# Kernel tuning notes

Hardware: AMD Instinct MI355X
Metric: run time of the kernel (lower is better)

## Reference

```python
import jax, jax.numpy as jnp
import numpy as np

EMBED = 1024
NUM_HEADS = 16
HEAD = EMBED // NUM_HEADS  # 64


def setup_inputs() -> dict:
    key = jax.random.key(0)
    kx, kk, kq, kv = jax.random.split(key, 4)
    B, T = 4, 4096
    scale = 1.0 / np.sqrt(EMBED)
    x = jax.random.normal(kx, (B, T, EMBED), dtype=jnp.float32)
    # nn.Linear(embed, head, bias=False) stores weight [head, embed]
    Wk = jax.random.normal(kk, (HEAD, EMBED), dtype=jnp.float32) * scale
    Wq = jax.random.normal(kq, (HEAD, EMBED), dtype=jnp.float32) * scale
    Wv = jax.random.normal(kv, (HEAD, EMBED), dtype=jnp.float32) * scale
    return {"x": x, "Wk": Wk, "Wq": Wq, "Wv": Wv}


def reference(x, Wk, Wq, Wv):
    # x: [B, T, C]; W*: [H, C] (torch Linear layout, y = x @ W.T)
    k = jnp.einsum('btc,hc->bth', x, Wk)  # [B, T, H]
    q = jnp.einsum('btc,hc->bth', x, Wq)
    v = jnp.einsum('btc,hc->bth', x, Wv)
    scale = k.shape[-1] ** -0.5
    wei = jnp.einsum('bth,bsh->bts', q, k) * scale  # [B, T, T]
    wei = jax.nn.softmax(wei, axis=-1)  # no causal mask in source
    out = jnp.einsum('bts,bsh->bth', wei, v)  # [B, T, H]
    return out
```

## Files before the change

kernel.cpp:

```cpp
#include <hip/hip_runtime.h>
#include <hip/hip_bf16.h>
#include <cstdint>

#define TSEQ 4096
#define NB   4
#define HD   64
#define CEMB 1024
#define NQ   8
#define KVCH (TSEQ / NQ)
#define NTOK (NB * TSEQ)
#define SCL  0.18033688011112042f
#define FM   16.0f

typedef __attribute__((ext_vector_type(8)))  short bfrag;
typedef __attribute__((ext_vector_type(4)))  float f4;
typedef __attribute__((ext_vector_type(16))) float f16v;

#define MFMA16(a, b, c) __builtin_amdgcn_mfma_f32_16x16x32_bf16(a, b, c, 0, 0, 0)
#define MFMA32(a, b, c) __builtin_amdgcn_mfma_f32_32x32x16_bf16(a, b, c, 0, 0, 0)

static __device__ __forceinline__ unsigned short f2bf(float f) {
    __hip_bfloat16 h = __float2bfloat16(f);
    return __builtin_bit_cast(unsigned short, h);
}

static __device__ __forceinline__ float bf2f(unsigned short u) {
    const unsigned v = (unsigned)u << 16;
    return __builtin_bit_cast(float, v);
}

static __device__ __forceinline__ unsigned cvtpk(float lo, float hi) {
    unsigned r;
    asm("v_cvt_pk_bf16_f32 %0, %1, %2" : "=v"(r) : "v"(lo), "v"(hi));
    return r;
}

static __device__ __forceinline__ bfrag cvt8pk(const float4 a, const float4 b) {
    uint4 o;
    o.x = cvtpk(a.x, a.y);
    o.y = cvtpk(a.z, a.w);
    o.z = cvtpk(b.x, b.y);
    o.w = cvtpk(b.z, b.w);
    return __builtin_bit_cast(bfrag, o);
}


__global__ __launch_bounds__(256) void wcvt_kernel(
    const float* __restrict__ Wq, const float* __restrict__ Wk,
    const float* __restrict__ Wv, unsigned short* __restrict__ wb)
{
    const int row = blockIdx.x;
    const int col = threadIdx.x * 4;
    const float* W = (row < 64) ? Wq + (size_t)row * CEMB
                   : (row < 128) ? Wk + (size_t)(row - 64) * CEMB
                   : Wv + (size_t)(row - 128) * CEMB;
    const float4 v = *reinterpret_cast<const float4*>(W + col);
    ushort4 o;
    o.x = f2bf(v.x); o.y = f2bf(v.y); o.z = f2bf(v.z); o.w = f2bf(v.w);
    *reinterpret_cast<ushort4*>(wb + (size_t)row * CEMB + col) = o;
}

__global__ __launch_bounds__(256) void proj_kernel(
    const float* __restrict__ x, const unsigned short* __restrict__ wb,
    unsigned short* __restrict__ qb, unsigned short* __restrict__ kf,
    unsigned short* __restrict__ vf)
{
    __shared__ __attribute__((aligned(16))) unsigned short xs[2][32 * 64];
    __shared__ __attribute__((aligned(16))) unsigned short ws[2][192 * 64];

    const int tid  = threadIdx.x;
    const int w    = tid >> 6;
    const int lane = tid & 63;
    const int ln15 = lane & 15, lg = lane >> 4;
    const int rowg = (w >> 1) * 16;
    const int colg = (w & 1) * 96;
    const int rowbase = blockIdx.x * 32;

    f4 acc[6];
    #pragma unroll
    for (int j = 0; j < 6; ++j) acc[j] = f4{0.f, 0.f, 0.f, 0.f};

    const int xrow = tid >> 3;
    const int xs8  = tid & 7;
    const int xswz = (xrow & 7) << 4;

    float4 xf0, xf1;
    bfrag  wf[6];
    auto LOADP = [&](int k0) {
        const float* xsrc = x + (size_t)(rowbase + xrow) * CEMB + k0 + xs8 * 8;
        xf0 = reinterpret_cast<const float4*>(xsrc)[0];
        xf1 = reinterpret_cast<const float4*>(xsrc)[1];
        #pragma unroll
        for (int i = 0; i < 6; ++i) {
            const int seg = tid + i * 256;
            const int srow = seg >> 3, sc = seg & 7;
            wf[i] = *reinterpret_cast<const bfrag*>(wb + (size_t)srow * CEMB + k0 + sc * 8);
        }
    };
    auto WRITEP = [&](int c) {
        char* xd = (char*)xs[c];
        char* wd = (char*)ws[c];
        const bfrag xb = cvt8pk(xf0, xf1);
        *reinterpret_cast<bfrag*>(xd + xrow * 128 + ((xs8 * 16) ^ xswz)) = xb;
        #pragma unroll
        for (int i = 0; i < 6; ++i) {
            const int seg = tid + i * 256;
            const int srow = seg >> 3, sc = seg & 7;
            *reinterpret_cast<bfrag*>(wd + srow * 128 + ((sc * 16) ^ ((srow & 7) << 4))) = wf[i];
        }
    };

    LOADP(0);
    WRITEP(0);
    __syncthreads();

    for (int ch = 0; ch < 16; ++ch) {
        const int c = ch & 1;
        if (ch < 15) LOADP((ch + 1) * 64);

        const char* xp = (const char*)xs[c];
        const char* wp = (const char*)ws[c];
        __builtin_amdgcn_s_setprio(1);
        #pragma unroll
        for (int ks = 0; ks < 2; ++ks) {
            const int cb = ks * 64 + lg * 16;
            const int r0 = rowg + ln15;
            const bfrag a0 = *reinterpret_cast<const bfrag*>(xp + r0 * 128 + (cb ^ ((r0 & 7) << 4)));
            #pragma unroll
            for (int ct = 0; ct < 6; ++ct) {
                const int wr = colg + ct * 16 + ln15;
                const bfrag b = *reinterpret_cast<const bfrag*>(wp + wr * 128 + (cb ^ ((wr & 7) << 4)));
                acc[ct] = MFMA16(a0, b, acc[ct]);
            }
        }
        __builtin_amdgcn_s_setprio(0);

        if (ch < 15) WRITEP(c ^ 1);
        __syncthreads();
    }

    #pragma unroll
    for (int ct = 0; ct < 6; ++ct) {
        const int c = colg + ct * 16 + ln15;
        #pragma unroll
        for (int r = 0; r < 4; ++r) {
            const int grow = rowbase + rowg + 4 * lg + r;
            const int bbi = grow >> 12, t = grow & 4095;
            const int tile = t >> 6, kvr = t & 63;
            if (c < 64) {
                qb[(size_t)grow * HD + c] = f2bf(acc[ct][r] * SCL);
            } else if (c < 128) {
                const int d = c - 64;
                const unsigned short bv16 = f2bf(acc[ct][r]);
                const int lane2 = (kvr & 31) + 32 * ((d >> 3) & 1);
                const size_t idx =
                    ((((size_t)bbi * 64 + tile) * 4 + (d >> 4)) * 2 + (kvr >> 5)) * 512
                    + lane2 * 8 + (d & 7);
                kf[idx] = bv16;
            } else {
                const int d = c - 128;
                const unsigned short bv16 = f2bf(acc[ct][r]);
                const int lane2 = (d & 31) + 32 * ((kvr >> 3) & 1);
                const size_t idx =
                    ((((size_t)bbi * 64 + tile) * 4 + (kvr >> 4)) * 2 + (d >> 5)) * 512
                    + lane2 * 8 + (kvr & 7);
                vf[idx] = bv16;
            }
        }
    }
}

__global__ __launch_bounds__(256, 3) void attn_kernel(
    const unsigned short* __restrict__ qb, const unsigned short* __restrict__ kf,
    const unsigned short* __restrict__ vf, uint2* __restrict__ po2,
    float* __restrict__ pl)
{
    const int w    = threadIdx.x >> 6;
    const int lane = threadIdx.x & 63;
    const int ql   = lane & 31;
    const int hi   = lane >> 5;
    const int chunk = blockIdx.x;
    const int xg    = blockIdx.y;
    const int q0   = xg * 128 + w * 32;
    const int bb   = xg >> 5;
    const int tbase = bb * 64 + chunk * 8;

    bfrag aq[4];
    #pragma unroll
    for (int s = 0; s < 4; ++s)
        aq[s] = *reinterpret_cast<const bfrag*>(
            qb + (size_t)(q0 + ql) * HD + 16 * s + 8 * hi);

    const unsigned short* kp = kf + (size_t)tbase * 4096 + lane * 8;
    const unsigned short* vp = vf + (size_t)tbase * 4096 + lane * 8;

    bfrag ka[4], kc[4], va[4], vc[4];
    auto LOADK = [&](int it) {
        const unsigned short* p = kp + (size_t)it * 4096;
        #pragma unroll
        for (int s = 0; s < 4; ++s) {
            ka[s] = *reinterpret_cast<const bfrag*>(p + (2 * s) * 512);
            kc[s] = *reinterpret_cast<const bfrag*>(p + (2 * s + 1) * 512);
        }
    };
    auto LOADV = [&](int it) {
        const unsigned short* p = vp + (size_t)it * 4096;
        #pragma unroll
        for (int s = 0; s < 4; ++s) {
            va[s] = *reinterpret_cast<const bfrag*>(p + (2 * s) * 512);
            vc[s] = *reinterpret_cast<const bfrag*>(p + (2 * s + 1) * 512);
        }
    };

    auto mkpa = [&](const f16v& p, const int u0) -> bfrag {
        unsigned a0 = cvtpk(p[4 * u0 + 0], p[4 * u0 + 1]);
        unsigned a1 = cvtpk(p[4 * u0 + 2], p[4 * u0 + 3]);
        unsigned b0 = cvtpk(p[4 * u0 + 4], p[4 * u0 + 5]);
        unsigned b1 = cvtpk(p[4 * u0 + 6], p[4 * u0 + 7]);
        asm("v_permlane32_swap_b32 %0, %1" : "+v"(a0), "+v"(b0));
        asm("v_permlane32_swap_b32 %0, %1" : "+v"(a1), "+v"(b1));
        const uint4 u = make_uint4(a0, a1, b0, b1);
        return __builtin_bit_cast(bfrag, u);
    };

    f16v o0, o1;
    #pragma unroll
    for (int i = 0; i < 16; ++i) { o0[i] = 0.f; o1[i] = 0.f; }
    float lsum = 0.f;

    const int NIT = KVCH / 64;
    LOADK(0);
    LOADV(0);

    for (int it = 0; it < NIT; ++it) {
        f16v s0v, s1v;
        #pragma unroll
        for (int i = 0; i < 16; ++i) { s0v[i] = -FM; s1v[i] = -FM; }
        __builtin_amdgcn_s_setprio(1);
        #pragma unroll
        for (int s = 0; s < 4; ++s) {
            s0v = MFMA32(ka[s], aq[s], s0v);
            s1v = MFMA32(kc[s], aq[s], s1v);
        }
        __builtin_amdgcn_s_setprio(0);
        if (it < NIT - 1) LOADK(it + 1);

        #pragma unroll
        for (int i = 0; i < 16; ++i) {
            s0v[i] = __builtin_amdgcn_exp2f(s0v[i]);
            s1v[i] = __builtin_amdgcn_exp2f(s1v[i]);
        }
        float a[16];
        #pragma unroll
        for (int i = 0; i < 16; ++i) a[i] = s0v[i] + s1v[i];
        #pragma unroll
        for (int st = 8; st > 0; st >>= 1)
            #pragma unroll
            for (int i = 0; i < 8; ++i) if (i < st) a[i] += a[i + st];
        lsum += a[0];

        const bfrag pa0 = mkpa(s0v, 0);
        const bfrag pa1 = mkpa(s0v, 2);
        const bfrag pa2 = mkpa(s1v, 0);
        const bfrag pa3 = mkpa(s1v, 2);

        __builtin_amdgcn_s_setprio(1);
        o0 = MFMA32(va[0], pa0, o0);  o1 = MFMA32(vc[0], pa0, o1);
        o0 = MFMA32(va[1], pa1, o0);  o1 = MFMA32(vc[1], pa1, o1);
        o0 = MFMA32(va[2], pa2, o0);  o1 = MFMA32(vc[2], pa2, o1);
        o0 = MFMA32(va[3], pa3, o0);  o1 = MFMA32(vc[3], pa3, o1);
        __builtin_amdgcn_s_setprio(0);
        if (it < NIT - 1) LOADV(it + 1);
    }

    lsum += __shfl_xor(lsum, 32);

    const int wid = chunk * 512 + xg * 4 + w;
    uint2* pw = po2 + ((size_t)wid * 8) * 64 + lane;
    #pragma unroll
    for (int u = 0; u < 4; ++u) {
        uint2 w0, w1;
        w0.x = cvtpk(o0[4 * u + 0], o0[4 * u + 1]);
        w0.y = cvtpk(o0[4 * u + 2], o0[4 * u + 3]);
        pw[(size_t)u * 64] = w0;
        w1.x = cvtpk(o1[4 * u + 0], o1[4 * u + 1]);
        w1.y = cvtpk(o1[4 * u + 2], o1[4 * u + 3]);
        pw[(size_t)(4 + u) * 64] = w1;
    }
    if (hi == 0) {
        pl[chunk * NTOK + q0 + ql] = lsum;
    }
}

__global__ __launch_bounds__(256) void merge_kernel(
    const uint2* __restrict__ po2, const float* __restrict__ pl,
    float* __restrict__ out)
{
    const int t   = blockIdx.x * 256 + threadIdx.x;
    const int row = t >> 4, d0 = (t & 15) * 4;
    const int xg = row >> 7, w = (row >> 5) & 3, ql = row & 31;
    const int h = d0 >> 5, u = (d0 >> 3) & 3, hi = (d0 >> 2) & 1;
    const int lane = ql + 32 * hi;
    const int slot = h * 4 + u;

    float lt = 0.f;
    f4 acc = {0.f, 0.f, 0.f, 0.f};
    #pragma unroll
    for (int q = 0; q < NQ; ++q) {
        lt += pl[q * NTOK + row];
        const int wid = q * 512 + xg * 4 + w;
        const uint2 v = po2[((size_t)wid * 8 + slot) * 64 + lane];
        acc[0] += bf2f((unsigned short)(v.x & 0xffffu));
        acc[1] += bf2f((unsigned short)(v.x >> 16));
        acc[2] += bf2f((unsigned short)(v.y & 0xffffu));
        acc[3] += bf2f((unsigned short)(v.y >> 16));
    }
    const float inv = 1.0f / lt;
    f4 r = { acc[0] * inv, acc[1] * inv, acc[2] * inv, acc[3] * inv };
    *reinterpret_cast<f4*>(out + (size_t)row * HD + d0) = r;
}

extern "C" void kernel_launch(void* const* d_in, const int* in_sizes, int n_in,
                              void* d_out, int out_size, void* d_ws, size_t ws_size,
                              hipStream_t stream) {
    (void)in_sizes; (void)n_in; (void)out_size; (void)ws_size;
    const float* x  = (const float*)d_in[0];
    const float* Wk = (const float*)d_in[1];
    const float* Wq = (const float*)d_in[2];
    const float* Wv = (const float*)d_in[3];

    unsigned short* qb = (unsigned short*)d_ws;
    unsigned short* kf = qb + (size_t)NTOK * HD;
    unsigned short* vf = kf + (size_t)NTOK * HD;
    unsigned short* wb = vf + (size_t)NTOK * HD;
    uint2* po2 = (uint2*)(wb + (size_t)192 * CEMB);
    float* pl  = (float*)(po2 + (size_t)NQ * 512 * 8 * 64);

    wcvt_kernel<<<192, 256, 0, stream>>>(Wq, Wk, Wv, wb);
    proj_kernel<<<512, 256, 0, stream>>>(x, wb, qb, kf, vf);
    attn_kernel<<<dim3(NQ, 128), 256, 0, stream>>>(qb, kf, vf, po2, pl);
    merge_kernel<<<NTOK * HD / 1024, 256, 0, stream>>>(po2, pl, (float*)d_out);
}
```

Measured before the change: 57.81 us.

## Stage K/V tiles through double-buffered LDS shared across block waves

Previously each of the four waves in a block loaded the same K and V tile fragments straight from global memory into registers. Now the block loads each 64-key K/V tile once cooperatively, with each thread fetching a quarter, stores it into a double-buffered LDS array, and every wave reads its MFMA operands from LDS. This cuts redundant global and L2 traffic by a factor of four. In exchange it adds two block barriers per iteration and LDS reads in the inner loop, which may serialize waves and limit latency hiding.

```diff
diff --git a/kernel.cpp b/kernel.cpp
--- a/kernel.cpp
+++ b/kernel.cpp
@@ -175,8 +175,12 @@
     const unsigned short* __restrict__ vf, uint2* __restrict__ po2,
     float* __restrict__ pl)
 {
-    const int w    = threadIdx.x >> 6;
-    const int lane = threadIdx.x & 63;
+    __shared__ __attribute__((aligned(16))) unsigned short kl[2][4096];
+    __shared__ __attribute__((aligned(16))) unsigned short vl[2][4096];
+
+    const int tid  = threadIdx.x;
+    const int w    = tid >> 6;
+    const int lane = tid & 63;
     const int ql   = lane & 31;
     const int hi   = lane >> 5;
     const int chunk = blockIdx.x;
@@ -191,25 +195,22 @@
         aq[s] = *reinterpret_cast<const bfrag*>(
             qb + (size_t)(q0 + ql) * HD + 16 * s + 8 * hi);
 
-    const unsigned short* kp = kf + (size_t)tbase * 4096 + lane * 8;
-    const unsigned short* vp = vf + (size_t)tbase * 4096 + lane * 8;
-
-    bfrag ka[4], kc[4], va[4], vc[4];
-    auto LOADK = [&](int it) {
-        const unsigned short* p = kp + (size_t)it * 4096;
-        #pragma unroll
-        for (int s = 0; s < 4; ++s) {
-            ka[s] = *reinterpret_cast<const bfrag*>(p + (2 * s) * 512);
-            kc[s] = *reinterpret_cast<const bfrag*>(p + (2 * s + 1) * 512);
-        }
-    };
-    auto LOADV = [&](int it) {
-        const unsigned short* p = vp + (size_t)it * 4096;
-        #pragma unroll
-        for (int s = 0; s < 4; ++s) {
-            va[s] = *reinterpret_cast<const bfrag*>(p + (2 * s) * 512);
-            vc[s] = *reinterpret_cast<const bfrag*>(p + (2 * s + 1) * 512);
-        }
+    const unsigned short* kg = kf + (size_t)tbase * 4096 + tid * 8;
+    const unsigned short* vg = vf + (size_t)tbase * 4096 + tid * 8;
+
+    bfrag sk0, sk1, sv0, sv1;
+    auto LOADT = [&](int it) {
+        const size_t o = (size_t)it * 4096;
+        sk0 = *reinterpret_cast<const bfrag*>(kg + o);
+        sk1 = *reinterpret_cast<const bfrag*>(kg + o + 2048);
+        sv0 = *reinterpret_cast<const bfrag*>(vg + o);
+        sv1 = *reinterpret_cast<const bfrag*>(vg + o + 2048);
+    };
+    auto WRITET = [&](int c) {
+        *reinterpret_cast<bfrag*>(&kl[c][tid * 8]) = sk0;
+        *reinterpret_cast<bfrag*>(&kl[c][2048 + tid * 8]) = sk1;
+        *reinterpret_cast<bfrag*>(&vl[c][tid * 8]) = sv0;
+        *reinterpret_cast<bfrag*>(&vl[c][2048 + tid * 8]) = sv1;
     };
 
     auto mkpa = [&](const f16v& p, const int u0) -> bfrag {
@@ -229,21 +230,29 @@
     float lsum = 0.f;
 
     const int NIT = KVCH / 64;
-    LOADK(0);
-    LOADV(0);
+    LOADT(0);
+    WRITET(0);
+    __syncthreads();
 
     for (int it = 0; it < NIT; ++it) {
+        const int c = it & 1;
+        if (it < NIT - 1) LOADT(it + 1);
+
+        const char* kbh = (const char*)&kl[c][0];
+        const char* vbh = (const char*)&vl[c][0];
+
         f16v s0v, s1v;
         #pragma unroll
         for (int i = 0; i < 16; ++i) { s0v[i] = -FM; s1v[i] = -FM; }
         __builtin_amdgcn_s_setprio(1);
         #pragma unroll
         for (int s = 0; s < 4; ++s) {
-            s0v = MFMA32(ka[s], aq[s], s0v);
-            s1v = MFMA32(kc[s], aq[s], s1v);
+            const bfrag ka = *reinterpret_cast<const bfrag*>(kbh + (2 * s) * 1024 + lane * 16);
+            const bfrag kc = *reinterpret_cast<const bfrag*>(kbh + (2 * s + 1) * 1024 + lane * 16);
+            s0v = MFMA32(ka, aq[s], s0v);
+            s1v = MFMA32(kc, aq[s], s1v);
         }
         __builtin_amdgcn_s_setprio(0);
-        if (it < NIT - 1) LOADK(it + 1);
 
         #pragma unroll
         for (int i = 0; i < 16; ++i) {
@@ -265,12 +274,27 @@
         const bfrag pa3 = mkpa(s1v, 2);
 
         __builtin_amdgcn_s_setprio(1);
-        o0 = MFMA32(va[0], pa0, o0);  o1 = MFMA32(vc[0], pa0, o1);
-        o0 = MFMA32(va[1], pa1, o0);  o1 = MFMA32(vc[1], pa1, o1);
-        o0 = MFMA32(va[2], pa2, o0);  o1 = MFMA32(vc[2], pa2, o1);
-        o0 = MFMA32(va[3], pa3, o0);  o1 = MFMA32(vc[3], pa3, o1);
+        {
+            const bfrag va0 = *reinterpret_cast<const bfrag*>(vbh + 0 * 1024 + lane * 16);
+            const bfrag vc0 = *reinterpret_cast<const bfrag*>(vbh + 1 * 1024 + lane * 16);
+            o0 = MFMA32(va0, pa0, o0);  o1 = MFMA32(vc0, pa0, o1);
+            const bfrag va1 = *reinterpret_cast<const bfrag*>(vbh + 2 * 1024 + lane * 16);
+            const bfrag vc1 = *reinterpret_cast<const bfrag*>(vbh + 3 * 1024 + lane * 16);
+            o0 = MFMA32(va1, pa1, o0);  o1 = MFMA32(vc1, pa1, o1);
+            const bfrag va2 = *reinterpret_cast<const bfrag*>(vbh + 4 * 1024 + lane * 16);
+            const bfrag vc2 = *reinterpret_cast<const bfrag*>(vbh + 5 * 1024 + lane * 16);
+            o0 = MFMA32(va2, pa2, o0);  o1 = MFMA32(vc2, pa2, o1);
+            const bfrag va3 = *reinterpret_cast<const bfrag*>(vbh + 6 * 1024 + lane * 16);
+            const bfrag vc3 = *reinterpret_cast<const bfrag*>(vbh + 7 * 1024 + lane * 16);
+            o0 = MFMA32(va3, pa3, o0);  o1 = MFMA32(vc3, pa3, o1);
+        }
         __builtin_amdgcn_s_setprio(0);
-        if (it < NIT - 1) LOADV(it + 1);
+
+        if (it < NIT - 1) {
+            __syncthreads();
+            WRITET(c ^ 1);
+            __syncthreads();
+        }
     }
 
     lsum += __shfl_xor(lsum, 32);
```

After: 54.86 us. -5.1%, faster.
